# Kernel optimization log

Hardware: AMD Instinct MI355X
Metric: run time of the kernel (lower is better)

The kernel has to match this reference:

```python
import jax, jax.numpy as jnp
import numpy as np

VOCAB = 400001  # vocab_size + 1
H = 100         # n_hidden
B = 512
T = 25
FC = 128
NC = 2
FORGET_BIAS = 1.0


def setup_inputs() -> dict:
    key = jax.random.key(0)
    ks = jax.random.split(key, 8)
    features = jax.random.randint(ks[0], (B, T), 0, VOCAB, dtype=jnp.int32)
    embedding = jax.random.normal(ks[1], (VOCAB, H), dtype=jnp.float32) * 0.05
    # BasicLSTMCell kernel: [input_dim + hidden, 4*hidden], gate order (i, j, f, o)
    k1 = jax.random.normal(ks[2], (2 * H, 4 * H), dtype=jnp.float32) * 0.05
    b1 = jnp.zeros((4 * H,), dtype=jnp.float32)
    k2 = jax.random.normal(ks[3], (2 * H, 4 * H), dtype=jnp.float32) * 0.05
    b2 = jnp.zeros((4 * H,), dtype=jnp.float32)
    w_fc1 = jax.random.normal(ks[4], (H, FC), dtype=jnp.float32) * 0.05
    b_fc1 = jnp.zeros((FC,), dtype=jnp.float32)
    w_fc2 = jax.random.normal(ks[5], (FC, NC), dtype=jnp.float32) * 0.05
    b_fc2 = jnp.zeros((NC,), dtype=jnp.float32)
    return {"features": features, "embedding": embedding,
            "k1": k1, "b1": b1, "k2": k2, "b2": b2,
            "w_fc1": w_fc1, "b_fc1": b_fc1, "w_fc2": w_fc2, "b_fc2": b_fc2}


def _lstm_cell(c, h, x, kernel, bias):
    z = jnp.concatenate([x, h], axis=-1) @ kernel + bias  # [B, 4H]
    i, j, f, o = jnp.split(z, 4, axis=-1)
    c_new = c * jax.nn.sigmoid(f + FORGET_BIAS) + jax.nn.sigmoid(i) * jnp.tanh(j)
    h_new = jnp.tanh(c_new) * jax.nn.sigmoid(o)
    return c_new, h_new


def reference(features, embedding, k1, b1, k2, b2, w_fc1, b_fc1, w_fc2, b_fc2):
    x = embedding[features]                      # [B, T, H]
    xs = jnp.swapaxes(x, 0, 1)                   # [T, B, H] for scan over time
    batch = features.shape[0]
    zeros = jnp.zeros((batch, H), dtype=embedding.dtype)

    def step(carry, xt):
        c1, h1, c2, h2 = carry
        c1, h1 = _lstm_cell(c1, h1, xt, k1, b1)
        c2, h2 = _lstm_cell(c2, h2, h1, k2, b2)
        return (c1, h1, c2, h2), None

    (c1, h1, c2, h2), _ = jax.lax.scan(step, (zeros, zeros, zeros, zeros), xs)
    # dynamic_rnn outputs[:, -1, :] == final top-layer hidden state h2
    fc1 = h2 @ w_fc1 + b_fc1                     # linear, no activation (tf.layers.dense default)
    pred = fc1 @ w_fc2 + b_fc2                   # [B, num_classes] logits
    return pred
```

## Files before the change

kernel.cpp:

```cpp
#include <hip/hip_runtime.h>
#include <cstdint>
#include <cstddef>

#define VOCABSZ 400001
#define Hn 100
#define Tn 25
#define Bn 512
#define FCn 128
#define Rr 2
#define NBLK (Bn / Rr)
#define NTHR 512

typedef _Float16 half2_t __attribute__((ext_vector_type(2)));

__device__ __forceinline__ half2_t h2bits(unsigned v) {
    union { unsigned u; half2_t h; } x; x.u = v; return x.h;
}
__device__ __forceinline__ float fdot2f(half2_t a, half2_t b, float c) {
    return __builtin_amdgcn_fdot2(a, b, c, false);
}
__device__ __forceinline__ float sigm(float x) {
    return __fdividef(1.0f, 1.0f + __expf(-x));
}
__device__ __forceinline__ float tanh_fast(float x) {
    float e = __expf(2.0f * x);
    return __fdividef(e - 1.0f, e + 1.0f);
}

__global__ void prep_weights(const float* __restrict__ k1,
                             const float* __restrict__ k2,
                             uint4* __restrict__ WP) {
    int t = blockIdx.x * blockDim.x + threadIdx.x;
    if (t >= 2 * 25 * 400) return;
    int l   = t / 10000;
    int rem = t % 10000;
    int kq  = rem / 400;
    int o   = rem % 400;
    int u = o >> 2, g = o & 3;
    int c = g * 100 + u;
    const float* K = l ? k2 : k1;
    union { unsigned u32; half2_t h; } d[4];
    #pragma unroll
    for (int j = 0; j < 4; j++) {
        int k0 = 8 * kq + 2 * j;
        d[j].h.x = (_Float16)K[(k0    ) * 400 + c];
        d[j].h.y = (_Float16)K[(k0 + 1) * 400 + c];
    }
    uint4 v; v.x = d[0].u32; v.y = d[1].u32; v.z = d[2].u32; v.w = d[3].u32;
    WP[t] = v;
}

__device__ __forceinline__ float lstm_update(float z, int g, float& cst) {
    float t1 = __shfl_xor(z, 1);
    float t2 = __shfl_xor(z, 2);
    float t3 = __shfl_xor(t1, 2);
    bool g0 = (g & 1) != 0, g1 = (g & 2) != 0;
    float vi = g1 ? (g0 ? t3 : t2) : (g0 ? t1 : z);
    float vj = g1 ? (g0 ? t2 : t3) : (g0 ? z  : t1);
    float vf = g1 ? (g0 ? t1 : z ) : (g0 ? t3 : t2);
    float vo = g1 ? (g0 ? z  : t1) : (g0 ? t2 : t3);
    cst = cst * sigm(vf + 1.0f) + sigm(vi) * tanh_fast(vj);
    return tanh_fast(cst) * sigm(vo);
}

#define GEMV_LAYER(SRC0, SRC1, LIDX, BIAS, Z0, Z1)                           \
  {                                                                          \
    const uint4* _p0 = (const uint4*)(SRC0);                                 \
    const uint4* _p1 = (const uint4*)(SRC1);                                 \
    uint4 _vx = _p0[lane < 25 ? lane : 0];                                   \
    uint4 _vy = _p1[lane < 25 ? lane : 0];                                   \
    float _a0=0.f,_a1=0.f,_a2=0.f,_a3=0.f;                                   \
    float _d0=0.f,_d1=0.f,_d2=0.f,_d3=0.f;                                   \
    _Pragma("unroll")                                                        \
    for (int kq = 0; kq < 25; kq++) {                                        \
      uint4 _w = w[LIDX][kq];                                                \
      unsigned _s0 = (unsigned)__builtin_amdgcn_readlane((int)_vx.x, kq);    \
      unsigned _s1 = (unsigned)__builtin_amdgcn_readlane((int)_vx.y, kq);    \
      unsigned _s2 = (unsigned)__builtin_amdgcn_readlane((int)_vx.z, kq);    \
      unsigned _s3 = (unsigned)__builtin_amdgcn_readlane((int)_vx.w, kq);    \
      _a0 = fdot2f(h2bits(_w.x), h2bits(_s0), _a0);                          \
      _a1 = fdot2f(h2bits(_w.y), h2bits(_s1), _a1);                          \
      _a2 = fdot2f(h2bits(_w.z), h2bits(_s2), _a2);                          \
      _a3 = fdot2f(h2bits(_w.w), h2bits(_s3), _a3);                          \
      unsigned _t0 = (unsigned)__builtin_amdgcn_readlane((int)_vy.x, kq);    \
      unsigned _t1 = (unsigned)__builtin_amdgcn_readlane((int)_vy.y, kq);    \
      unsigned _t2 = (unsigned)__builtin_amdgcn_readlane((int)_vy.z, kq);    \
      unsigned _t3 = (unsigned)__builtin_amdgcn_readlane((int)_vy.w, kq);    \
      _d0 = fdot2f(h2bits(_w.x), h2bits(_t0), _d0);                          \
      _d1 = fdot2f(h2bits(_w.y), h2bits(_t1), _d1);                          \
      _d2 = fdot2f(h2bits(_w.z), h2bits(_t2), _d2);                          \
      _d3 = fdot2f(h2bits(_w.w), h2bits(_t3), _d3);                          \
    }                                                                        \
    Z0 = _a0 + _a1 + _a2 + _a3 + (BIAS);                                     \
    Z1 = _d0 + _d1 + _d2 + _d3 + (BIAS);                                     \
  }

__global__ __launch_bounds__(NTHR, 2) void lstm_main(
    const int*   __restrict__ features,
    const float* __restrict__ embedding,
    const float* __restrict__ b1,
    const float* __restrict__ b2,
    const float* __restrict__ w_fc1,
    const float* __restrict__ b_fc1,
    const float* __restrict__ w_fc2,
    const float* __restrict__ b_fc2,
    const uint4* __restrict__ WP,
    float*       __restrict__ out)
{
    __shared__ _Float16 xh1[Rr][200];
    __shared__ _Float16 xh2[Rr][200];
    __shared__ float    wred[8][2];

    const int tid  = threadIdx.x;
    const int lane = tid & 63;
    const int o    = (tid < 400) ? tid : 399;
    const int u = o >> 2, g = o & 3;
    const int c = g * 100 + u;
    const bool owner = (tid < 400);

    uint4 w[2][25];
    #pragma unroll
    for (int l = 0; l < 2; l++)
        #pragma unroll
        for (int kq = 0; kq < 25; kq++)
            w[l][kq] = WP[(l * 25 + kq) * 400 + o];

    const float bias1 = b1[c];
    const float bias2 = b2[c];

    if (tid < 200) {
        int r = tid / 100, uu = tid % 100;
        xh1[r][100 + uu] = (_Float16)0.0f;
        xh2[r][uu]       = (_Float16)0.0f;
        xh2[r][100 + uu] = (_Float16)0.0f;
    }
    if (tid < 100) {
        int r = tid / 50, p = tid % 50;
        int f0 = features[(blockIdx.x * Rr + r) * Tn + 0];
        float2 e = *(const float2*)(embedding + (size_t)f0 * Hn + 2 * p);
        half2_t h; h.x = (_Float16)e.x; h.y = (_Float16)e.y;
        ((half2_t*)&xh1[r][0])[p] = h;
    }
    __syncthreads();

    float c1[Rr] = {0.f, 0.f}, c2[Rr] = {0.f, 0.f};
    float h1v[Rr] = {0.f, 0.f}, h2v[Rr] = {0.f, 0.f};

    for (int step = 0; step < Tn; step++) {
        float2 epre = {0.f, 0.f};
        int prow = 0, pp = 0;
        if (tid < 448) {
            if (owner && g == 1 && step + 1 < Tn) {
                prow = (u >= 50);
                pp   = u % 50;
                int f1 = features[(blockIdx.x * Rr + prow) * Tn + step + 1];
                epre = *(const float2*)(embedding + (size_t)f1 * Hn + 2 * pp);
            }
            float z0, z1;
            GEMV_LAYER(&xh1[0][0], &xh1[1][0], 0, bias1, z0, z1);
            h1v[0] = lstm_update(z0, g, c1[0]);
            h1v[1] = lstm_update(z1, g, c1[1]);
        }
        __syncthreads();
        if (owner) {
            if (g == 0) {
                xh1[0][100 + u] = (_Float16)h1v[0];
                xh1[1][100 + u] = (_Float16)h1v[1];
                xh2[0][u]       = (_Float16)h1v[0];
                xh2[1][u]       = (_Float16)h1v[1];
            }
            if (g == 1 && step + 1 < Tn) {
                half2_t h; h.x = (_Float16)epre.x; h.y = (_Float16)epre.y;
                ((half2_t*)&xh1[prow][0])[pp] = h;
            }
        }
        __syncthreads();
        if (tid < 448) {
            float z0, z1;
            GEMV_LAYER(&xh2[0][0], &xh2[1][0], 1, bias2, z0, z1);
            h2v[0] = lstm_update(z0, g, c2[0]);
            h2v[1] = lstm_update(z1, g, c2[1]);
        }
        __syncthreads();
        if (owner && g == 0) {
            xh2[0][100 + u] = (_Float16)h2v[0];
            xh2[1][100 + u] = (_Float16)h2v[1];
        }
    }
    __syncthreads();

    if (tid < Rr * FCn) {
        int r = tid >> 7;
        int j = tid & 127;
        float acc = b_fc1[j];
        #pragma unroll 10
        for (int uu = 0; uu < Hn; uu++)
            acc = fmaf((float)xh2[r][100 + uu], w_fc1[uu * FCn + j], acc);
        float p0 = acc * w_fc2[2 * j + 0];
        float p1 = acc * w_fc2[2 * j + 1];
        #pragma unroll
        for (int off = 32; off > 0; off >>= 1) {
            p0 += __shfl_down(p0, off, 64);
            p1 += __shfl_down(p1, off, 64);
        }
        if (lane == 0) {
            int wv = tid >> 6;
            wred[wv][0] = p0;
            wred[wv][1] = p1;
        }
    }
    __syncthreads();
    if (tid < 4) {
        int r = tid >> 1, cls = tid & 1;
        out[(blockIdx.x * Rr + r) * 2 + cls] =
            wred[2 * r][cls] + wred[2 * r + 1][cls] + b_fc2[cls];
    }
}

extern "C" void kernel_launch(void* const* d_in, const int* in_sizes, int n_in,
                              void* d_out, int out_size, void* d_ws, size_t ws_size,
                              hipStream_t stream) {
    const int*   features  = (const int*)  d_in[0];
    const float* embedding = (const float*)d_in[1];
    const float* k1        = (const float*)d_in[2];
    const float* b1        = (const float*)d_in[3];
    const float* k2        = (const float*)d_in[4];
    const float* b2        = (const float*)d_in[5];
    const float* w_fc1     = (const float*)d_in[6];
    const float* b_fc1     = (const float*)d_in[7];
    const float* w_fc2     = (const float*)d_in[8];
    const float* b_fc2     = (const float*)d_in[9];

    uint4* WP = (uint4*)d_ws;

    prep_weights<<<(20000 + 255) / 256, 256, 0, stream>>>(k1, k2, WP);
    lstm_main<<<NBLK, NTHR, 0, stream>>>(features, embedding, b1, b2,
                                         w_fc1, b_fc1, w_fc2, b_fc2,
                                         WP, (float*)d_out);
}
```

Measured before the change: 344.1 us.

## Replace per-row fdot2 GEMV with MFMA 16x16x32 over 16-row batch tiles

The kernel now processes 16 batch rows per block (32 blocks) and computes each LSTM layer's gate preactivations with MFMA f16 16x16x32 instructions, reading weight fragments from a tile-packed global buffer every step instead of keeping them in registers. Shared hidden-state buffers are double-buffered with padded pitch, and the embedding prefetch and FC head are restructured. This trades register-resident weights and 256-block parallelism for matrix-core throughput and fewer barriers per row, at the risk of low CU occupancy and repeated weight reloads from cache each timestep.

```diff
diff --git a/kernel.cpp b/kernel.cpp
--- a/kernel.cpp
+++ b/kernel.cpp
@@ -2,23 +2,20 @@
 #include <cstdint>
 #include <cstddef>
 
-#define VOCABSZ 400001
 #define Hn 100
 #define Tn 25
 #define Bn 512
 #define FCn 128
-#define Rr 2
-#define NBLK (Bn / Rr)
+#define ROWS 16
+#define NBLK (Bn / ROWS)
 #define NTHR 512
-
-typedef _Float16 half2_t __attribute__((ext_vector_type(2)));
-
-__device__ __forceinline__ half2_t h2bits(unsigned v) {
-    union { unsigned u; half2_t h; } x; x.u = v; return x.h;
-}
-__device__ __forceinline__ float fdot2f(half2_t a, half2_t b, float c) {
-    return __builtin_amdgcn_fdot2(a, b, c, false);
-}
+#define PITCH 232
+#define KPAD 224
+
+typedef _Float16 v8h __attribute__((ext_vector_type(8)));
+typedef float    v4f __attribute__((ext_vector_type(4)));
+union U4H8 { uint4 u; v8h h; };
+
 __device__ __forceinline__ float sigm(float x) {
     return __fdividef(1.0f, 1.0f + __expf(-x));
 }
@@ -29,71 +26,97 @@
 
 __global__ void prep_weights(const float* __restrict__ k1,
                              const float* __restrict__ k2,
-                             uint4* __restrict__ WP) {
-    int t = blockIdx.x * blockDim.x + threadIdx.x;
-    if (t >= 2 * 25 * 400) return;
-    int l   = t / 10000;
-    int rem = t % 10000;
-    int kq  = rem / 400;
-    int o   = rem % 400;
-    int u = o >> 2, g = o & 3;
+                             uint4* __restrict__ WB) {
+    int t = blockIdx.x * 256 + threadIdx.x;
+    if (t >= 2 * 25 * 7 * 64) return;
+    int lane = t & 63;
+    int rest = t >> 6;
+    int kk   = rest % 7;
+    int tile = (rest / 7) % 25;
+    int l    = rest / (7 * 25);
+    int q = lane >> 4, n = lane & 15;
+    int colp = tile * 16 + n;
+    int u = colp >> 2, g = colp & 3;
     int c = g * 100 + u;
+    int k0 = kk * 32 + q * 8;
     const float* K = l ? k2 : k1;
-    union { unsigned u32; half2_t h; } d[4];
+    union { unsigned u32; _Float16 h[2]; } d[4];
     #pragma unroll
     for (int j = 0; j < 4; j++) {
-        int k0 = 8 * kq + 2 * j;
-        d[j].h.x = (_Float16)K[(k0    ) * 400 + c];
-        d[j].h.y = (_Float16)K[(k0 + 1) * 400 + c];
+        int ka = k0 + 2 * j, kb = ka + 1;
+        d[j].h[0] = (_Float16)((ka < 200) ? K[ka * 400 + c] : 0.0f);
+        d[j].h[1] = (_Float16)((kb < 200) ? K[kb * 400 + c] : 0.0f);
     }
     uint4 v; v.x = d[0].u32; v.y = d[1].u32; v.z = d[2].u32; v.w = d[3].u32;
-    WP[t] = v;
-}
-
-__device__ __forceinline__ float lstm_update(float z, int g, float& cst) {
-    float t1 = __shfl_xor(z, 1);
-    float t2 = __shfl_xor(z, 2);
-    float t3 = __shfl_xor(t1, 2);
-    bool g0 = (g & 1) != 0, g1 = (g & 2) != 0;
-    float vi = g1 ? (g0 ? t3 : t2) : (g0 ? t1 : z);
-    float vj = g1 ? (g0 ? t2 : t3) : (g0 ? z  : t1);
-    float vf = g1 ? (g0 ? t1 : z ) : (g0 ? t3 : t2);
-    float vo = g1 ? (g0 ? z  : t1) : (g0 ? t2 : t3);
-    cst = cst * sigm(vf + 1.0f) + sigm(vi) * tanh_fast(vj);
-    return tanh_fast(cst) * sigm(vo);
-}
-
-#define GEMV_LAYER(SRC0, SRC1, LIDX, BIAS, Z0, Z1)                           \
-  {                                                                          \
-    const uint4* _p0 = (const uint4*)(SRC0);                                 \
-    const uint4* _p1 = (const uint4*)(SRC1);                                 \
-    uint4 _vx = _p0[lane < 25 ? lane : 0];                                   \
-    uint4 _vy = _p1[lane < 25 ? lane : 0];                                   \
-    float _a0=0.f,_a1=0.f,_a2=0.f,_a3=0.f;                                   \
-    float _d0=0.f,_d1=0.f,_d2=0.f,_d3=0.f;                                   \
-    _Pragma("unroll")                                                        \
-    for (int kq = 0; kq < 25; kq++) {                                        \
-      uint4 _w = w[LIDX][kq];                                                \
-      unsigned _s0 = (unsigned)__builtin_amdgcn_readlane((int)_vx.x, kq);    \
-      unsigned _s1 = (unsigned)__builtin_amdgcn_readlane((int)_vx.y, kq);    \
-      unsigned _s2 = (unsigned)__builtin_amdgcn_readlane((int)_vx.z, kq);    \
-      unsigned _s3 = (unsigned)__builtin_amdgcn_readlane((int)_vx.w, kq);    \
-      _a0 = fdot2f(h2bits(_w.x), h2bits(_s0), _a0);                          \
-      _a1 = fdot2f(h2bits(_w.y), h2bits(_s1), _a1);                          \
-      _a2 = fdot2f(h2bits(_w.z), h2bits(_s2), _a2);                          \
-      _a3 = fdot2f(h2bits(_w.w), h2bits(_s3), _a3);                          \
-      unsigned _t0 = (unsigned)__builtin_amdgcn_readlane((int)_vy.x, kq);    \
-      unsigned _t1 = (unsigned)__builtin_amdgcn_readlane((int)_vy.y, kq);    \
-      unsigned _t2 = (unsigned)__builtin_amdgcn_readlane((int)_vy.z, kq);    \
-      unsigned _t3 = (unsigned)__builtin_amdgcn_readlane((int)_vy.w, kq);    \
-      _d0 = fdot2f(h2bits(_w.x), h2bits(_t0), _d0);                          \
-      _d1 = fdot2f(h2bits(_w.y), h2bits(_t1), _d1);                          \
-      _d2 = fdot2f(h2bits(_w.z), h2bits(_t2), _d2);                          \
-      _d3 = fdot2f(h2bits(_w.w), h2bits(_t3), _d3);                          \
-    }                                                                        \
-    Z0 = _a0 + _a1 + _a2 + _a3 + (BIAS);                                     \
-    Z1 = _d0 + _d1 + _d2 + _d3 + (BIAS);                                     \
-  }
+    WB[t] = v;
+}
+
+template<int NT>
+__device__ __forceinline__ void layer_phase(
+    const uint4* __restrict__ WBl,
+    const _Float16* __restrict__ xsrc,
+    _Float16* __restrict__ dstA, int offA,
+    _Float16* __restrict__ dstB, int offB,
+    const float* __restrict__ bl,
+    float* __restrict__ cst,
+    int wv, int lane)
+{
+    const int q = lane >> 4, n = lane & 15;
+    const int g = n & 3, v = n >> 2;
+
+    U4H8 bf[NT][7];
+    #pragma unroll
+    for (int i = 0; i < NT; i++) {
+        int t = 8 * i + wv;
+        #pragma unroll
+        for (int kk = 0; kk < 7; kk++)
+            bf[i][kk].u = WBl[(t * 7 + kk) * 64 + lane];
+    }
+    U4H8 af[7];
+    #pragma unroll
+    for (int kk = 0; kk < 7; kk++)
+        af[kk].u = *(const uint4*)(xsrc + n * PITCH + kk * 32 + q * 8);
+
+    #pragma unroll
+    for (int i = 0; i < NT; i++) {
+        v4f acc = { bl[i], bl[i], bl[i], bl[i] };
+        #pragma unroll
+        for (int kk = 0; kk < 7; kk++)
+            acc = __builtin_amdgcn_mfma_f32_16x16x32_f16(af[kk].h, bf[i][kk].h, acc, 0, 0, 0);
+
+        float a0 = acc[0], a1 = acc[1], a2 = acc[2], a3 = acc[3];
+        bool gb0 = (g & 1) != 0, gb1 = (g & 2) != 0;
+        float selA  = gb0 ? a1 : a0;
+        float selB  = gb0 ? a3 : a2;
+        float selA1 = gb0 ? a0 : a1;
+        float selB1 = gb0 ? a2 : a3;
+        float s0 = gb1 ? selB  : selA;
+        float s1 = gb1 ? selB1 : selA1;
+        float s2 = gb1 ? selA  : selB;
+        float s3 = gb1 ? selA1 : selB1;
+        float w0 = s0;
+        float w1 = __shfl_xor(s1, 1);
+        float w2 = __shfl_xor(s2, 2);
+        float w3 = __shfl_xor(s3, 3);
+        float p01 = gb0 ? w1 : w0;
+        float p10 = gb0 ? w0 : w1;
+        float p23 = gb0 ? w3 : w2;
+        float p32 = gb0 ? w2 : w3;
+        float zi = gb1 ? p23 : p01;
+        float zj = gb1 ? p32 : p10;
+        float zf = gb1 ? p01 : p23;
+        float zo = gb1 ? p10 : p32;
+
+        float cn = cst[i] * sigm(zf + 1.0f) + sigm(zi) * tanh_fast(zj);
+        cst[i] = cn;
+        float h = tanh_fast(cn) * sigm(zo);
+
+        int row = 4 * q + g;
+        int uu  = 4 * (8 * i + wv) + v;
+        dstA[row * PITCH + offA + uu] = (_Float16)h;
+        if (dstB) dstB[row * PITCH + offB + uu] = (_Float16)h;
+    }
+}
 
 __global__ __launch_bounds__(NTHR, 2) void lstm_main(
     const int*   __restrict__ features,
@@ -104,116 +127,106 @@
     const float* __restrict__ b_fc1,
     const float* __restrict__ w_fc2,
     const float* __restrict__ b_fc2,
-    const uint4* __restrict__ WP,
+    const uint4* __restrict__ WB,
     float*       __restrict__ out)
 {
-    __shared__ _Float16 xh1[Rr][200];
-    __shared__ _Float16 xh2[Rr][200];
-    __shared__ float    wred[8][2];
+    __shared__ alignas(16) _Float16 xh1[2][ROWS][PITCH];
+    __shared__ alignas(16) _Float16 xh2[2][ROWS][PITCH];
 
     const int tid  = threadIdx.x;
     const int lane = tid & 63;
-    const int o    = (tid < 400) ? tid : 399;
-    const int u = o >> 2, g = o & 3;
-    const int c = g * 100 + u;
-    const bool owner = (tid < 400);
-
-    uint4 w[2][25];
-    #pragma unroll
-    for (int l = 0; l < 2; l++)
-        #pragma unroll
-        for (int kq = 0; kq < 25; kq++)
-            w[l][kq] = WP[(l * 25 + kq) * 400 + o];
-
-    const float bias1 = b1[c];
-    const float bias2 = b2[c];
-
-    if (tid < 200) {
-        int r = tid / 100, uu = tid % 100;
-        xh1[r][100 + uu] = (_Float16)0.0f;
-        xh2[r][uu]       = (_Float16)0.0f;
-        xh2[r][100 + uu] = (_Float16)0.0f;
-    }
-    if (tid < 100) {
-        int r = tid / 50, p = tid % 50;
-        int f0 = features[(blockIdx.x * Rr + r) * Tn + 0];
-        float2 e = *(const float2*)(embedding + (size_t)f0 * Hn + 2 * p);
-        half2_t h; h.x = (_Float16)e.x; h.y = (_Float16)e.y;
-        ((half2_t*)&xh1[r][0])[p] = h;
+    const int wv   = tid >> 6;
+    const int n    = lane & 15;
+    const int g    = n & 3, v = n >> 2;
+    const int blk  = blockIdx.x;
+
+    const uint4* WB1 = WB;
+    const uint4* WB2 = WB + 25 * 7 * 64;
+
+    const int NTw = (wv == 0) ? 4 : 3;
+    float bl1[4] = {0, 0, 0, 0}, bl2[4] = {0, 0, 0, 0};
+    for (int i = 0; i < NTw; i++) {
+        int t  = 8 * i + wv;
+        int cc = g * 100 + (4 * t + v);
+        bl1[i] = b1[cc];
+        bl2[i] = b2[cc];
+    }
+    float c1[4] = {0, 0, 0, 0}, c2[4] = {0, 0, 0, 0};
+
+    {
+        unsigned* p1 = (unsigned*)&xh1[0][0][0];
+        unsigned* p2 = (unsigned*)&xh2[0][0][0];
+        const int ndw = 2 * ROWS * PITCH / 2;
+        for (int i = tid; i < ndw; i += NTHR) { p1[i] = 0u; p2[i] = 0u; }
+    }
+    const int rowx = tid / 25, px = tid % 25;
+    if (tid < 400) {
+        int f0 = features[(blk * ROWS + rowx) * Tn + 0];
+        float4 e = *(const float4*)(embedding + (size_t)f0 * Hn + 4 * px);
+        union { _Float16 h[4]; uint2 u; } pk;
+        pk.h[0] = (_Float16)e.x; pk.h[1] = (_Float16)e.y;
+        pk.h[2] = (_Float16)e.z; pk.h[3] = (_Float16)e.w;
+        *(uint2*)&xh1[0][rowx][4 * px] = pk.u;
     }
     __syncthreads();
 
-    float c1[Rr] = {0.f, 0.f}, c2[Rr] = {0.f, 0.f};
-    float h1v[Rr] = {0.f, 0.f}, h2v[Rr] = {0.f, 0.f};
-
-    for (int step = 0; step < Tn; step++) {
-        float2 epre = {0.f, 0.f};
-        int prow = 0, pp = 0;
-        if (tid < 448) {
-            if (owner && g == 1 && step + 1 < Tn) {
-                prow = (u >= 50);
-                pp   = u % 50;
-                int f1 = features[(blockIdx.x * Rr + prow) * Tn + step + 1];
-                epre = *(const float2*)(embedding + (size_t)f1 * Hn + 2 * pp);
-            }
-            float z0, z1;
-            GEMV_LAYER(&xh1[0][0], &xh1[1][0], 0, bias1, z0, z1);
-            h1v[0] = lstm_update(z0, g, c1[0]);
-            h1v[1] = lstm_update(z1, g, c1[1]);
-        }
+    for (int t = 0; t < Tn; t++) {
+        const int cur = t & 1, nxt = cur ^ 1;
+
+        float4 xp = {0, 0, 0, 0};
+        const bool hasx = (tid < 400) && (t + 1 < Tn);
+        if (hasx) {
+            int f = features[(blk * ROWS + rowx) * Tn + t + 1];
+            xp = *(const float4*)(embedding + (size_t)f * Hn + 4 * px);
+        }
+
+        if (wv == 0)
+            layer_phase<4>(WB1, &xh1[cur][0][0], &xh1[nxt][0][0], 100,
+                           &xh2[cur][0][0], 0, bl1, c1, wv, lane);
+        else
+            layer_phase<3>(WB1, &xh1[cur][0][0], &xh1[nxt][0][0], 100,
+                           &xh2[cur][0][0], 0, bl1, c1, wv, lane);
         __syncthreads();
-        if (owner) {
-            if (g == 0) {
-                xh1[0][100 + u] = (_Float16)h1v[0];
-                xh1[1][100 + u] = (_Float16)h1v[1];
-                xh2[0][u]       = (_Float16)h1v[0];
-                xh2[1][u]       = (_Float16)h1v[1];
-            }
-            if (g == 1 && step + 1 < Tn) {
-                half2_t h; h.x = (_Float16)epre.x; h.y = (_Float16)epre.y;
-                ((half2_t*)&xh1[prow][0])[pp] = h;
-            }
+
+        if (wv == 0)
+            layer_phase<4>(WB2, &xh2[cur][0][0], &xh2[nxt][0][0], 100,
+                           (_Float16*)nullptr, 0, bl2, c2, wv, lane);
+        else
+            layer_phase<3>(WB2, &xh2[cur][0][0], &xh2[nxt][0][0], 100,
+                           (_Float16*)nullptr, 0, bl2, c2, wv, lane);
+
+        if (hasx) {
+            union { _Float16 h[4]; uint2 u; } pk;
+            pk.h[0] = (_Float16)xp.x; pk.h[1] = (_Float16)xp.y;
+            pk.h[2] = (_Float16)xp.z; pk.h[3] = (_Float16)xp.w;
+            *(uint2*)&xh1[nxt][rowx][4 * px] = pk.u;
         }
         __syncthreads();
-        if (tid < 448) {
-            float z0, z1;
-            GEMV_LAYER(&xh2[0][0], &xh2[1][0], 1, bias2, z0, z1);
-            h2v[0] = lstm_update(z0, g, c2[0]);
-            h2v[1] = lstm_update(z1, g, c2[1]);
-        }
-        __syncthreads();
-        if (owner && g == 0) {
-            xh2[0][100 + u] = (_Float16)h2v[0];
-            xh2[1][100 + u] = (_Float16)h2v[1];
-        }
-    }
-    __syncthreads();
-
-    if (tid < Rr * FCn) {
-        int r = tid >> 7;
-        int j = tid & 127;
-        float acc = b_fc1[j];
-        #pragma unroll 10
-        for (int uu = 0; uu < Hn; uu++)
-            acc = fmaf((float)xh2[r][100 + uu], w_fc1[uu * FCn + j], acc);
-        float p0 = acc * w_fc2[2 * j + 0];
-        float p1 = acc * w_fc2[2 * j + 1];
+    }
+
+    const _Float16* h2base = &xh2[Tn & 1][0][0];
+    #pragma unroll
+    for (int rr = 0; rr < 2; rr++) {
+        int row = 2 * wv + rr;
+        float acc0 = b_fc1[lane];
+        float acc1 = b_fc1[lane + 64];
+        const _Float16* hp = h2base + row * PITCH + 100;
+        for (int u = 0; u < Hn; u++) {
+            float hv = (float)hp[u];
+            acc0 = fmaf(hv, w_fc1[u * FCn + lane], acc0);
+            acc1 = fmaf(hv, w_fc1[u * FCn + lane + 64], acc1);
+        }
+        float p0 = acc0 * w_fc2[2 * lane + 0] + acc1 * w_fc2[2 * (lane + 64) + 0];
+        float p1 = acc0 * w_fc2[2 * lane + 1] + acc1 * w_fc2[2 * (lane + 64) + 1];
         #pragma unroll
         for (int off = 32; off > 0; off >>= 1) {
-            p0 += __shfl_down(p0, off, 64);
-            p1 += __shfl_down(p1, off, 64);
+            p0 += __shfl_down(p0, off);
+            p1 += __shfl_down(p1, off);
         }
         if (lane == 0) {
-            int wv = tid >> 6;
-            wred[wv][0] = p0;
-            wred[wv][1] = p1;
-        }
-    }
-    __syncthreads();
-    if (tid < 4) {
-        int r = tid >> 1, cls = tid & 1;
-        out[(blockIdx.x * Rr + r) * 2 + cls] =
-            wred[2 * r][cls] + wred[2 * r + 1][cls] + b_fc2[cls];
+            out[(blk * ROWS + row) * 2 + 0] = p0 + b_fc2[0];
+            out[(blk * ROWS + row) * 2 + 1] = p1 + b_fc2[1];
+        }
     }
 }
 
@@ -231,10 +244,10 @@
     const float* w_fc2     = (const float*)d_in[8];
     const float* b_fc2     = (const float*)d_in[9];
 
-    uint4* WP = (uint4*)d_ws;
-
-    prep_weights<<<(20000 + 255) / 256, 256, 0, stream>>>(k1, k2, WP);
+    uint4* WBp = (uint4*)d_ws;
+
+    prep_weights<<<(2 * 25 * 7 * 64 + 255) / 256, 256, 0, stream>>>(k1, k2, WBp);
     lstm_main<<<NBLK, NTHR, 0, stream>>>(features, embedding, b1, b2,
                                          w_fc1, b_fc1, w_fc2, b_fc2,
-                                         WP, (float*)d_out);
-}
+                                         WBp, (float*)d_out);
+}
```

New measurement: 483.8 us. 40.6% more time.
